# Optimization experiments

Measured on AMD Instinct MI355X. Metric: run time of the kernel, lower is better.

## Reference

```python
import jax, jax.numpy as jnp
from jax import lax
import numpy as np

D, E, N, L = 192, 384, 16, 2
P_SZ, IMG, C_IN, K = 16, 224, 3, 3
NP = (IMG // P_SZ) ** 2          # 196 patches
M = NP + 1                        # +cls token
BATCH = 8


def setup_inputs() -> dict:
    key = jax.random.key(0)
    ks = iter(jax.random.split(key, 40))
    nrm = lambda shape, s=0.02: jax.random.normal(next(ks), shape, jnp.float32) * s
    inp = {
        "img": jax.random.normal(next(ks), (BATCH, C_IN, IMG, IMG), jnp.float32),
        "patch_w": nrm((C_IN * P_SZ * P_SZ, D)),
        "patch_b": jnp.zeros((D,), jnp.float32),
        "cls": jnp.zeros((1, 1, D), jnp.float32),
        "pos": nrm((1, M, D)),
        # per-layer stacked params (leading dim L)
        "ln_g": jnp.ones((L, D), jnp.float32), "ln_b": jnp.zeros((L, D), jnp.float32),
        "Wx": nrm((L, D, E)), "bx": jnp.zeros((L, E), jnp.float32),
        "Wz": nrm((L, D, E)), "bz": jnp.zeros((L, E), jnp.float32),
        "cwf": nrm((L, E, 1, K), 0.1), "cbf": jnp.zeros((L, E), jnp.float32),
        "cwb": nrm((L, E, 1, K), 0.1), "cbb": jnp.zeros((L, E), jnp.float32),
        "WBf": nrm((L, E, E * N)), "bBf": jnp.zeros((L, E * N), jnp.float32),
        "WCf": nrm((L, E, E * N)), "bCf": jnp.zeros((L, E * N), jnp.float32),
        "WDf": jnp.zeros((L, E, E), jnp.float32), "bDf": jnp.zeros((L, E), jnp.float32),
        "Af": nrm((L, E, N), 0.01), "dbf": jnp.zeros((L, E), jnp.float32),
        "WBb": nrm((L, E, E * N)), "bBb": jnp.zeros((L, E * N), jnp.float32),
        "WCb": nrm((L, E, E * N)), "bCb": jnp.zeros((L, E * N), jnp.float32),
        "WDb": jnp.zeros((L, E, E), jnp.float32), "bDb": jnp.zeros((L, E), jnp.float32),
        "Ab": nrm((L, E, N), 0.01), "dbb": jnp.zeros((L, E), jnp.float32),
        "Wout": nrm((L, E, D)), "bout": jnp.zeros((L, D), jnp.float32),
        "ng": jnp.ones((D,), jnp.float32), "nb": jnp.zeros((D,), jnp.float32),
    }
    return inp


def layernorm(x, g, b, eps=1e-5):
    mu = x.mean(-1, keepdims=True)
    var = ((x - mu) ** 2).mean(-1, keepdims=True)
    return (x - mu) * lax.rsqrt(var + eps) * g + b


def dwconv(x, w, b):
    # x: (B, M, E), w: (E, 1, K) depthwise, 'same' padding
    xc = jnp.transpose(x, (0, 2, 1))  # (B, E, M)
    pad = (w.shape[-1] - 1) // 2
    y = lax.conv_general_dilated(xc, w, (1,), [(pad, pad)],
                                 dimension_numbers=("NCH", "OIH", "NCH"),
                                 feature_group_count=w.shape[0])
    return jnp.transpose(y, (0, 2, 1)) + b


def ssm_recurrence(A, Bm, Cm, x):
    # A,Bm,Cm: (B,M,E,N); x: (B,M,E). Log-space prefix-product scan.
    eps = 1e-6
    signA = jnp.sign(A)
    absA = jnp.clip(jnp.abs(A), eps)
    logP = jnp.cumsum(jnp.log(absA), axis=1)
    P = jnp.cumprod(signA, axis=1) * jnp.exp(logP)
    invP = 1.0 / (P + eps)
    S = jnp.cumsum(invP * Bm * x[..., None], axis=1)
    h = P * S
    return (h * Cm).sum(-1)  # (B, M, E)


def vim_block(x, p, i):
    Bsz, Mseq, _ = x.shape
    xn = layernorm(x, p["ln_g"][i], p["ln_b"][i])
    xp = xn @ p["Wx"][i] + p["bx"][i]
    z = xn @ p["Wz"][i] + p["bz"][i]
    xf = jax.nn.silu(dwconv(xp, p["cwf"][i], p["cbf"][i]))
    xb = jax.nn.silu(dwconv(xp[:, ::-1], p["cwb"][i], p["cbb"][i])[:, ::-1])

    def branch(xs, WB, bB, WC, bC, WD, bD, Apar, db):
        Bm = (xs @ WB + bB).reshape(Bsz, Mseq, E, N)
        Cm = (xs @ WC + bC).reshape(Bsz, Mseq, E, N)
        Delta = jax.nn.softplus(xs @ WD + bD + db)          # (B,M,E)
        Afull = Delta[..., None] * Apar[None, None]          # (B,M,E,N)
        Bfull = Delta[..., None] * Bm
        return ssm_recurrence(Afull, Bfull, Cm, xs)

    y_f = branch(xf, p["WBf"][i], p["bBf"][i], p["WCf"][i], p["bCf"][i],
                 p["WDf"][i], p["bDf"][i], p["Af"][i], p["dbf"][i])
    y_b = branch(xb, p["WBb"][i], p["bBb"][i], p["WCb"][i], p["bCb"][i],
                 p["WDb"][i], p["bDb"][i], p["Ab"][i], p["dbb"][i])
    g = jax.nn.silu(z)
    y = (y_f + y_b) * g
    return y @ p["Wout"][i] + p["bout"][i] + x


def reference(img, patch_w, patch_b, cls, pos, ln_g, ln_b, Wx, bx, Wz, bz,
              cwf, cbf, cwb, cbb, WBf, bBf, WCf, bCf, WDf, bDf, Af, dbf,
              WBb, bBb, WCb, bCb, WDb, bDb, Ab, dbb, Wout, bout, ng, nb):
    Bsz = img.shape[0]
    hn = IMG // P_SZ
    # patchify (equivalent to Conv2d kernel=stride=patch): (B,3,H,W)->(B,NP,3*p*p)
    patches = img.reshape(Bsz, C_IN, hn, P_SZ, hn, P_SZ)
    patches = patches.transpose(0, 2, 4, 1, 3, 5).reshape(Bsz, NP, C_IN * P_SZ * P_SZ)
    x = patches @ patch_w + patch_b                           # (B,NP,D)
    x = jnp.concatenate([jnp.broadcast_to(cls, (Bsz, 1, D)), x], axis=1)
    x = x + pos
    p = dict(ln_g=ln_g, ln_b=ln_b, Wx=Wx, bx=bx, Wz=Wz, bz=bz, cwf=cwf, cbf=cbf,
             cwb=cwb, cbb=cbb, WBf=WBf, bBf=bBf, WCf=WCf, bCf=bCf, WDf=WDf,
             bDf=bDf, Af=Af, dbf=dbf, WBb=WBb, bBb=bBb, WCb=WCb, bCb=bCb,
             WDb=WDb, bDb=bDb, Ab=Ab, dbb=dbb, Wout=Wout, bout=bout)
    for i in range(L):
        x = vim_block(x, p, i)
    return layernorm(x, ng, nb)  # (B, M, D)
```

## Files before the change

### kernel.cpp

```cpp
#include <hip/hip_runtime.h>
#include <hip/hip_bf16.h>
#include <math.h>

#define BATCH   8
#define C_IN    3
#define IMG_SZ  224
#define P_SZ    16
#define NPATCH  196
#define MSEQ    197
#define DDIM    192
#define EDIM    384
#define NSTATE  16
#define ENDIM   (EDIM*NSTATE)
#define LLAYERS 2
#define ROWS    (BATCH*MSEQ)
#define PROWS   (BATCH*NPATCH)
#define PATCH_K (C_IN*P_SZ*P_SZ)
#define AP_ROWS 1664

typedef unsigned short u16;
typedef __attribute__((ext_vector_type(8))) short bf16x8;
typedef __attribute__((ext_vector_type(16))) float f32x16;

__device__ __forceinline__ float silu_f(float x) { return x / (1.f + expf(-x)); }

__device__ __forceinline__ u16 f2bf(float f) {
    unsigned u = __float_as_uint(f);
    unsigned r = (u + 0x7FFFu + ((u >> 16) & 1u)) >> 16;
    return (u16)r;
}
__device__ __forceinline__ float bf2f(u16 h) {
    return __uint_as_float(((unsigned)h) << 16);
}

__global__ __launch_bounds__(256) void patchify_k(const float* __restrict__ img,
                                                  float* __restrict__ out) {
    int idx = blockIdx.x * 256 + threadIdx.x;
    if (idx >= PROWS * PATCH_K) return;
    int r = idx / PATCH_K, col = idx - r * PATCH_K;
    int b = r / NPATCH, p = r - b * NPATCH;
    int ph = p / 14, pw = p - ph * 14;
    int c = col >> 8, rem = col & 255, py = rem >> 4, px = rem & 15;
    out[idx] = img[((b * C_IN + c) * IMG_SZ + ph * P_SZ + py) * IMG_SZ + pw * P_SZ + px];
}

__global__ __launch_bounds__(256) void assemble_k(const float* __restrict__ xemb,
                                                  const float* __restrict__ cls,
                                                  const float* __restrict__ pos,
                                                  float* __restrict__ x) {
    int idx = blockIdx.x * 256 + threadIdx.x;
    if (idx >= ROWS * DDIM) return;
    int d = idx % DDIM;
    int bm = idx / DDIM;
    int m = bm % MSEQ, b = bm / MSEQ;
    float v;
    if (m == 0) v = cls[d];
    else        v = xemb[((b * NPATCH) + (m - 1)) * DDIM + d];
    x[idx] = v + pos[m * DDIM + d];
}

__global__ __launch_bounds__(256) void layernorm_k(const float* __restrict__ x,
                                                   const float* __restrict__ g,
                                                   const float* __restrict__ b,
                                                   float* __restrict__ o, int nrows) {
    int wave = threadIdx.x >> 6;
    int lane = threadIdx.x & 63;
    int row = blockIdx.x * 4 + wave;
    if (row >= nrows) return;
    const float* xr = x + (long)row * DDIM;
    float v0 = xr[lane], v1 = xr[lane + 64], v2 = xr[lane + 128];
    float s = v0 + v1 + v2;
    #pragma unroll
    for (int off = 1; off < 64; off <<= 1) s += __shfl_xor(s, off);
    float mu = s * (1.f / 192.f);
    float d0 = v0 - mu, d1 = v1 - mu, d2 = v2 - mu;
    float q = d0 * d0 + d1 * d1 + d2 * d2;
    #pragma unroll
    for (int off = 1; off < 64; off <<= 1) q += __shfl_xor(q, off);
    float inv = rsqrtf(q * (1.f / 192.f) + 1e-5f);
    float* orow = o + (long)row * DDIM;
    orow[lane]       = d0 * inv * g[lane]       + b[lane];
    orow[lane + 64]  = d1 * inv * g[lane + 64]  + b[lane + 64];
    orow[lane + 128] = d2 * inv * g[lane + 128] + b[lane + 128];
}

__global__ __launch_bounds__(256) void convA_k(const float* __restrict__ xf,
                                               const float* __restrict__ xb,
                                               u16* __restrict__ Af3,
                                               u16* __restrict__ Ab3) {
    int idx = blockIdx.x * 256 + threadIdx.x;
    if (idx >= ROWS * EDIM) return;
    int row = idx / EDIM, k = idx - row * EDIM;
    long base = (long)row * EDIM + k;
    #pragma unroll
    for (int s = 0; s < 2; ++s) {
        float x = s ? xb[idx] : xf[idx];
        u16* out = s ? Ab3 : Af3;
        u16 hb = f2bf(x);        float fh = bf2f(hb);
        float r1 = x - fh;
        u16 mb = f2bf(r1);       float fm = bf2f(mb);
        u16 lb = f2bf(r1 - fm);
        out[base] = hb;
        out[(long)AP_ROWS * EDIM + base] = mb;
        out[2L * AP_ROWS * EDIM + base] = lb;
    }
}

__global__ __launch_bounds__(256) void convWt_k(const float* __restrict__ W0,
                                                const float* __restrict__ W1,
                                                const float* __restrict__ W2,
                                                const float* __restrict__ W3,
                                                u16* __restrict__ Wt) {
    int z = blockIdx.z;
    const float* W = (z == 0) ? W0 : (z == 1) ? W1 : (z == 2) ? W2 : W3;
    u16* out = Wt + (long)z * 3L * ENDIM * EDIM;
    __shared__ float tile[64][65];
    int n0 = blockIdx.x * 64, k0 = blockIdx.y * 64;
    int t = threadIdx.x;
    #pragma unroll
    for (int i = 0; i < 16; ++i) {
        int id = t + 256 * i;
        int kk = id >> 6, nn = id & 63;
        tile[kk][nn] = W[(long)(k0 + kk) * ENDIM + n0 + nn];
    }
    __syncthreads();
    #pragma unroll
    for (int i = 0; i < 2; ++i) {
        int id = t + 256 * i;
        int nn = id >> 3, ch = id & 7;
        uint4 hq, mq, lq;
        u16* hp = (u16*)&hq; u16* mp = (u16*)&mq; u16* lp = (u16*)&lq;
        #pragma unroll
        for (int j = 0; j < 8; ++j) {
            float x = tile[ch * 8 + j][nn];
            u16 hb = f2bf(x);        float fh = bf2f(hb);
            float r1 = x - fh;
            u16 mb = f2bf(r1);       float fm = bf2f(mb);
            u16 lb = f2bf(r1 - fm);
            hp[j] = hb; mp[j] = mb; lp[j] = lb;
        }
        long rowoff = (long)(n0 + nn) * EDIM + k0 + ch * 8;
        *(uint4*)&out[rowoff] = hq;
        *(uint4*)&out[(long)ENDIM * EDIM + rowoff] = mq;
        *(uint4*)&out[2L * ENDIM * EDIM + rowoff] = lq;
    }
}

__global__ __launch_bounds__(256) void gemm_mfma(
        const u16* __restrict__ A3,
        const u16* __restrict__ Wt0, const float* __restrict__ b0, float* __restrict__ C0,
        const u16* __restrict__ Wt1, const float* __restrict__ b1, float* __restrict__ C1) {
    const u16* Wt    = blockIdx.z ? Wt1 : Wt0;
    const float* bias = blockIdx.z ? b1 : b0;
    float* C          = blockIdx.z ? C1 : C0;
    __shared__ u16 As[3][128][40];
    int t = threadIdx.x;
    int lane = t & 63, wv = t >> 6;
    int wr = wv >> 1, wc = wv & 1;
    int l31 = lane & 31, l5 = lane >> 5;
    int rowBase = blockIdx.y * 128;
    long colBase = (long)blockIdx.x * 128;
    f32x16 acc[2][2] = {};

    for (int k0 = 0; k0 < EDIM; k0 += 32) {
        #pragma unroll
        for (int i = 0; i < 6; ++i) {
            int id = t + 256 * i;
            int p = id >> 9, rem = id & 511, row = rem >> 2, ch = rem & 3;
            const u16* src = A3 + ((long)p * AP_ROWS + rowBase + row) * EDIM + k0 + ch * 8;
            uint4 v = *(const uint4*)src;
            *(uint4*)&As[p][row][ch * 8] = v;
        }
        __syncthreads();
        bf16x8 af[2][2][3], wf[2][2][3];
        #pragma unroll
        for (int ks = 0; ks < 2; ++ks) {
            #pragma unroll
            for (int r = 0; r < 2; ++r)
                #pragma unroll
                for (int p = 0; p < 3; ++p)
                    af[ks][r][p] = *(const bf16x8*)&As[p][wr * 64 + r * 32 + l31][ks * 16 + l5 * 8];
            #pragma unroll
            for (int c = 0; c < 2; ++c)
                #pragma unroll
                for (int p = 0; p < 3; ++p)
                    wf[ks][c][p] = *(const bf16x8*)&Wt[((long)p * ENDIM + colBase + wc * 64 + c * 32 + l31) * EDIM
                                                      + k0 + ks * 16 + l5 * 8];
        }
        #pragma unroll
        for (int ks = 0; ks < 2; ++ks)
            #pragma unroll
            for (int r = 0; r < 2; ++r)
                #pragma unroll
                for (int c = 0; c < 2; ++c) {
                    f32x16 d = acc[r][c];
                    d = __builtin_amdgcn_mfma_f32_32x32x16_bf16(af[ks][r][0], wf[ks][c][0], d, 0, 0, 0);
                    d = __builtin_amdgcn_mfma_f32_32x32x16_bf16(af[ks][r][0], wf[ks][c][1], d, 0, 0, 0);
                    d = __builtin_amdgcn_mfma_f32_32x32x16_bf16(af[ks][r][1], wf[ks][c][0], d, 0, 0, 0);
                    d = __builtin_amdgcn_mfma_f32_32x32x16_bf16(af[ks][r][0], wf[ks][c][2], d, 0, 0, 0);
                    d = __builtin_amdgcn_mfma_f32_32x32x16_bf16(af[ks][r][2], wf[ks][c][0], d, 0, 0, 0);
                    d = __builtin_amdgcn_mfma_f32_32x32x16_bf16(af[ks][r][1], wf[ks][c][1], d, 0, 0, 0);
                    acc[r][c] = d;
                }
        __syncthreads();
    }
    #pragma unroll
    for (int r = 0; r < 2; ++r) {
        int rb = rowBase + wr * 64 + r * 32 + 4 * l5;
        #pragma unroll
        for (int c = 0; c < 2; ++c) {
            long cb = colBase + wc * 64 + c * 32 + l31;
            float bv = bias[cb];
            #pragma unroll
            for (int i = 0; i < 16; ++i) {
                int rr = rb + (i & 3) + 8 * (i >> 2);
                if (rr < ROWS) C[(long)rr * ENDIM + cb] = acc[r][c][i] + bv;
            }
        }
    }
}

#define SBK 16
template<bool SP, bool HASB2, bool HASRES>
__global__ __launch_bounds__(64) void gemm_s(const float* __restrict__ A0,
                                             const float* __restrict__ W0,
                                             const float* __restrict__ b10,
                                             const float* __restrict__ b20,
                                             const float* __restrict__ r0,
                                             float* __restrict__ C0,
                                             const float* __restrict__ A1,
                                             const float* __restrict__ W1,
                                             const float* __restrict__ b11,
                                             const float* __restrict__ b21,
                                             const float* __restrict__ r1,
                                             float* __restrict__ C1,
                                             int M, int N, int K) {
    const float* A  = blockIdx.z ? A1  : A0;
    const float* W  = blockIdx.z ? W1  : W0;
    const float* bp = blockIdx.z ? b11 : b10;
    const float* b2 = blockIdx.z ? b21 : b20;
    const float* rp = blockIdx.z ? r1  : r0;
    float*       C  = blockIdx.z ? C1  : C0;
    __shared__ float As[2][SBK][36];
    __shared__ float Wsh[2][SBK][36];
    int t = threadIdx.x;
    int tx = t & 7, ty = t >> 3;
    int rowBase = blockIdx.y * 32;
    long colBase = (long)blockIdx.x * 32;
    int rA = t >> 2, kqA = (t & 3) << 2;
    int kW = t >> 3, nqW = (t & 7) << 2;
    float acc[4][4] = {};
    int r0i = rowBase + rA, r1i = r0i + 16;

    auto loadA = [&](int k0, float4& a0, float4& a1) {
        a0 = make_float4(0.f,0.f,0.f,0.f); a1 = a0;
        if (r0i < M) a0 = *(const float4*)&A[(long)r0i * K + k0 + kqA];
        if (r1i < M) a1 = *(const float4*)&A[(long)r1i * K + k0 + kqA];
    };
    auto stage = [&](int buf, float4 a0, float4 a1, float4 w0, float4 w1) {
        As[buf][kqA + 0][rA] = a0.x; As[buf][kqA + 1][rA] = a0.y;
        As[buf][kqA + 2][rA] = a0.z; As[buf][kqA + 3][rA] = a0.w;
        As[buf][kqA + 0][rA + 16] = a1.x; As[buf][kqA + 1][rA + 16] = a1.y;
        As[buf][kqA + 2][rA + 16] = a1.z; As[buf][kqA + 3][rA + 16] = a1.w;
        *(float4*)&Wsh[buf][kW][nqW]     = w0;
        *(float4*)&Wsh[buf][kW + 8][nqW] = w1;
    };
    auto compute = [&](int buf) {
        #pragma unroll
        for (int kk = 0; kk < SBK; ++kk) {
            float4 av = *(const float4*)&As[buf][kk][ty << 2];
            float4 wv = *(const float4*)&Wsh[buf][kk][tx << 2];
            float ar[4] = {av.x, av.y, av.z, av.w};
            float wr[4] = {wv.x, wv.y, wv.z, wv.w};
            #pragma unroll
            for (int i = 0; i < 4; ++i)
                #pragma unroll
                for (int j = 0; j < 4; ++j) acc[i][j] += ar[i] * wr[j];
        }
    };

    {
        float4 a0, a1;
        loadA(0, a0, a1);
        float4 w0 = *(const float4*)&W[(long)kW * N + colBase + nqW];
        float4 w1 = *(const float4*)&W[(long)(kW + 8) * N + colBase + nqW];
        stage(0, a0, a1, w0, w1);
    }
    __syncthreads();
    int cur = 0;
    int nt = K / SBK;
    for (int kt = 1; kt < nt; ++kt) {
        int k0 = kt * SBK;
        float4 a0, a1;
        loadA(k0, a0, a1);
        float4 w0 = *(const float4*)&W[(long)(k0 + kW) * N + colBase + nqW];
        float4 w1 = *(const float4*)&W[(long)(k0 + kW + 8) * N + colBase + nqW];
        compute(cur);
        stage(cur ^ 1, a0, a1, w0, w1);
        __syncthreads();
        cur ^= 1;
    }
    compute(cur);

    #pragma unroll
    for (int i = 0; i < 4; ++i) {
        int r = rowBase + (ty << 2) + i;
        if (r >= M) break;
        long cb = colBase + (tx << 2);
        float vv[4];
        #pragma unroll
        for (int j = 0; j < 4; ++j) {
            float v = acc[i][j] + bp[cb + j];
            if (HASB2) v += b2[cb + j];
            if (SP) {
                double vd = (double)v;
                v = (float)(log1p(exp(-fabs(vd))) + fmax(vd, 0.0));
            }
            if (HASRES) v += rp[(long)r * N + cb + j];
            vv[j] = v;
        }
        float4 o; o.x = vv[0]; o.y = vv[1]; o.z = vv[2]; o.w = vv[3];
        *(float4*)&C[(long)r * N + cb] = o;
    }
}

__global__ __launch_bounds__(256) void dwconv_k(const float* __restrict__ xp,
                                                const float* __restrict__ wf,
                                                const float* __restrict__ bf,
                                                const float* __restrict__ wb,
                                                const float* __restrict__ bb,
                                                float* __restrict__ xf,
                                                float* __restrict__ xb) {
    int idx = blockIdx.x * 256 + threadIdx.x;
    if (idx >= ROWS * EDIM) return;
    int e = idx % EDIM;
    int bm = idx / EDIM;
    int m = bm % MSEQ, b = bm / MSEQ;
    const float* base = xp + (long)b * MSEQ * EDIM + e;
    float xm1 = (m > 0)        ? base[(m - 1) * EDIM] : 0.f;
    float x0  =                  base[m * EDIM];
    float xp1 = (m < MSEQ - 1) ? base[(m + 1) * EDIM] : 0.f;
    float f = wf[e * 3 + 0] * xm1 + wf[e * 3 + 1] * x0 + wf[e * 3 + 2] * xp1 + bf[e];
    float r = wb[e * 3 + 0] * xp1 + wb[e * 3 + 1] * x0 + wb[e * 3 + 2] * xm1 + bb[e];
    xf[idx] = silu_f(f);
    xb[idx] = silu_f(r);
}

__global__ __launch_bounds__(256) void ssm_scan_k(const float* __restrict__ Bm,
                                                  const float* __restrict__ Cm,
                                                  const float* __restrict__ Dlt,
                                                  const float* __restrict__ xs,
                                                  const float* __restrict__ Apar,
                                                  float* __restrict__ y,
                                                  const float* __restrict__ yother,
                                                  const float* __restrict__ zg,
                                                  float* __restrict__ ycomb) {
#pragma clang fp contract(off)
    __shared__ float lgP[MSEQ][17];
    __shared__ float trm[MSEQ][17];
    __shared__ signed char sgn[MSEQ][17];
    int be = blockIdx.x;
    int b = be / EDIM, e = be - b * EDIM;
    int t = threadIdx.x;
    int n0 = t & 15;
    float Ap = Apar[e * NSTATE + n0];
    const long dxBase = (long)b * MSEQ * EDIM + e;
    const long bcBase = (long)b * MSEQ * ENDIM + e * NSTATE;

    for (int idx = t; idx < MSEQ * NSTATE; idx += 256) {
        int m = idx >> 4;
        float delta = Dlt[dxBase + (long)m * EDIM];
        float A = delta * Ap;
        float sa = (A > 0.f) ? 1.f : ((A < 0.f) ? -1.f : 0.f);
        float absA = fmaxf(fabsf(A), 1e-6f);
        lgP[m][n0] = (float)log((double)absA);
        sgn[m][n0] = (signed char)sa;
    }
    __syncthreads();
    if (t < NSTATE) {
        float cl = 0.f, cs = 1.f;
        for (int m = 0; m < MSEQ; ++m) {
            float sa = (float)sgn[m][t];
            cs = cs * sa;
            cl = cl + lgP[m][t];
            lgP[m][t] = cl;
            sgn[m][t] = (signed char)cs;
        }
    }
    __syncthreads();
    for (int idx = t; idx < MSEQ * NSTATE; idx += 256) {
        int m = idx >> 4;
        float cl = lgP[m][n0];
        float cs = (float)sgn[m][n0];
        float ex = (float)exp((double)cl);
        float P = cs * ex;
        float tt = P + 1e-6f;
        float invP = 1.0f / tt;
        float delta = Dlt[dxBase + (long)m * EDIM];
        float xv = xs[dxBase + (long)m * EDIM];
        float Bv = Bm[bcBase + (long)m * ENDIM + n0];
        float Bfull = delta * Bv;
        float t1 = invP * Bfull;
        float t2 = t1 * xv;
        trm[m][n0] = t2;
        lgP[m][n0] = P;
    }
    __syncthreads();
    if (t < NSTATE) {
        float S = 0.f;
        for (int m = 0; m < MSEQ; ++m) {
            S = S + trm[m][t];
            float h = lgP[m][t] * S;
            trm[m][t] = h;
        }
    }
    __syncthreads();
    for (int m = t; m < MSEQ; m += 256) {
        const float* cp = &Cm[bcBase + (long)m * ENDIM];
        float a[16];
        #pragma unroll
        for (int n = 0; n < 16; ++n) a[n] = trm[m][n] * cp[n];
        float b0 = a[0] + a[8],  b1 = a[1] + a[9];
        float b2v = a[2] + a[10], b3 = a[3] + a[11];
        float b4 = a[4] + a[12], b5 = a[5] + a[13];
        float b6 = a[6] + a[14], b7 = a[7] + a[15];
        float c0 = b0 + b1, c2 = b2v + b3, c4 = b4 + b5, c6 = b6 + b7;
        float d0 = c0 + c2, d4 = c4 + c6;
        float val = d0 + d4;
        long o = dxBase + (long)m * EDIM;
        if (ycomb) ycomb[o] = (yother[o] + val) * silu_f(zg[o]);
        else       y[o] = val;
    }
}

extern "C" void kernel_launch(void* const* d_in, const int* in_sizes, int n_in,
                              void* d_out, int out_size, void* d_ws, size_t ws_size,
                              hipStream_t stream) {
    const float* img     = (const float*)d_in[0];
    const float* patch_w = (const float*)d_in[1];
    const float* patch_b = (const float*)d_in[2];
    const float* cls     = (const float*)d_in[3];
    const float* pos     = (const float*)d_in[4];
    const float* ln_g    = (const float*)d_in[5];
    const float* ln_b    = (const float*)d_in[6];
    const float* Wx  = (const float*)d_in[7];  const float* bx  = (const float*)d_in[8];
    const float* Wz  = (const float*)d_in[9];  const float* bz  = (const float*)d_in[10];
    const float* cwf = (const float*)d_in[11]; const float* cbf = (const float*)d_in[12];
    const float* cwb = (const float*)d_in[13]; const float* cbb = (const float*)d_in[14];
    const float* WBf = (const float*)d_in[15]; const float* bBf = (const float*)d_in[16];
    const float* WCf = (const float*)d_in[17]; const float* bCf = (const float*)d_in[18];
    const float* WDf = (const float*)d_in[19]; const float* bDf = (const float*)d_in[20];
    const float* Af  = (const float*)d_in[21]; const float* dbf = (const float*)d_in[22];
    const float* WBb = (const float*)d_in[23]; const float* bBb = (const float*)d_in[24];
    const float* WCb = (const float*)d_in[25]; const float* bCb = (const float*)d_in[26];
    const float* WDb = (const float*)d_in[27]; const float* bDb = (const float*)d_in[28];
    const float* Ab  = (const float*)d_in[29]; const float* dbb = (const float*)d_in[30];
    const float* Wout= (const float*)d_in[31]; const float* bout= (const float*)d_in[32];
    const float* ng  = (const float*)d_in[33]; const float* nb  = (const float*)d_in[34];

    float* ws = (float*)d_ws;
    float* xA   = ws;
    float* xB   = xA  + (size_t)ROWS * DDIM;
    float* xn   = xB  + (size_t)ROWS * DDIM;
    float* xp   = xn  + (size_t)ROWS * DDIM;
    float* zb   = xp  + (size_t)ROWS * EDIM;
    float* xfb  = zb  + (size_t)ROWS * EDIM;
    float* xbb  = xfb + (size_t)ROWS * EDIM;
    float* yfb  = xbb + (size_t)ROWS * EDIM;
    float* ybb  = yfb + (size_t)ROWS * EDIM;
    float* ycb  = ybb + (size_t)ROWS * EDIM;
    float* dlt  = ycb + (size_t)ROWS * EDIM;
    float* dlt2 = dlt + (size_t)ROWS * EDIM;
    float* Bmb  = dlt2 + (size_t)ROWS * EDIM;
    float* Cmb  = Bmb + (size_t)ROWS * ENDIM;
    u16*   Af3  = (u16*)(Cmb + (size_t)ROWS * ENDIM);
    u16*   Ab3  = Af3 + 3L * AP_ROWS * EDIM;
    u16*   Wt4  = Ab3 + 3L * AP_ROWS * EDIM;
    float* patches = Bmb;
    float* xemb    = Bmb + (size_t)PROWS * PATCH_K;

    const long WtSz = 3L * ENDIM * EDIM;

    patchify_k<<<(PROWS * PATCH_K + 255) / 256, 256, 0, stream>>>(img, patches);
    {
        dim3 g(DDIM / 32, (PROWS + 31) / 32, 1);
        gemm_s<false, false, false><<<g, 64, 0, stream>>>(
            patches, patch_w, patch_b, nullptr, nullptr, xemb,
            patches, patch_w, patch_b, nullptr, nullptr, xemb,
            PROWS, DDIM, PATCH_K);
    }
    assemble_k<<<(ROWS * DDIM + 255) / 256, 256, 0, stream>>>(xemb, cls, pos, xA);

    float* cur = xA; float* nxt = xB;
    for (int i = 0; i < LLAYERS; ++i) {
        layernorm_k<<<(ROWS + 3) / 4, 256, 0, stream>>>(cur, ln_g + i * DDIM, ln_b + i * DDIM, xn, ROWS);
        {
            dim3 g(EDIM / 32, (ROWS + 31) / 32, 2);
            gemm_s<false, false, false><<<g, 64, 0, stream>>>(
                xn, Wx + (size_t)i * DDIM * EDIM, bx + i * EDIM, nullptr, nullptr, xp,
                xn, Wz + (size_t)i * DDIM * EDIM, bz + i * EDIM, nullptr, nullptr, zb,
                ROWS, EDIM, DDIM);
        }
        dwconv_k<<<(ROWS * EDIM + 255) / 256, 256, 0, stream>>>(xp, cwf + i * EDIM * 3, cbf + i * EDIM,
                                                                cwb + i * EDIM * 3, cbb + i * EDIM, xfb, xbb);
        convA_k<<<(ROWS * EDIM + 255) / 256, 256, 0, stream>>>(xfb, xbb, Af3, Ab3);
        {
            dim3 g(EDIM / 32, (ROWS + 31) / 32, 2);
            gemm_s<true, true, false><<<g, 64, 0, stream>>>(
                xfb, WDf + (size_t)i * EDIM * EDIM, bDf + i * EDIM, dbf + i * EDIM, nullptr, dlt,
                xbb, WDb + (size_t)i * EDIM * EDIM, bDb + i * EDIM, dbb + i * EDIM, nullptr, dlt2,
                ROWS, EDIM, EDIM);
        }
        {
            dim3 g(ENDIM / 64, EDIM / 64, 4);
            convWt_k<<<g, 256, 0, stream>>>(
                WBf + (size_t)i * EDIM * ENDIM, WCf + (size_t)i * EDIM * ENDIM,
                WBb + (size_t)i * EDIM * ENDIM, WCb + (size_t)i * EDIM * ENDIM, Wt4);
        }
        {
            dim3 g(ENDIM / 128, AP_ROWS / 128, 2);
            gemm_mfma<<<g, 256, 0, stream>>>(
                Af3,
                Wt4 + 0 * WtSz, bBf + i * ENDIM, Bmb,
                Wt4 + 1 * WtSz, bCf + i * ENDIM, Cmb);
        }
        ssm_scan_k<<<BATCH * EDIM, 256, 0, stream>>>(Bmb, Cmb, dlt, xfb, Af + i * EDIM * NSTATE,
                                                     yfb, nullptr, nullptr, nullptr);
        {
            dim3 g(ENDIM / 128, AP_ROWS / 128, 2);
            gemm_mfma<<<g, 256, 0, stream>>>(
                Ab3,
                Wt4 + 2 * WtSz, bBb + i * ENDIM, Bmb,
                Wt4 + 3 * WtSz, bCb + i * ENDIM, Cmb);
        }
        ssm_scan_k<<<BATCH * EDIM, 256, 0, stream>>>(Bmb, Cmb, dlt2, xbb, Ab + i * EDIM * NSTATE,
                                                     ybb, yfb, zb, ycb);
        {
            dim3 g(DDIM / 32, (ROWS + 31) / 32, 1);
            gemm_s<false, false, true><<<g, 64, 0, stream>>>(
                ycb, Wout + (size_t)i * EDIM * DDIM, bout + i * DDIM, nullptr, cur, nxt,
                ycb, Wout + (size_t)i * EDIM * DDIM, bout + i * DDIM, nullptr, cur, nxt,
                ROWS, DDIM, EDIM);
        }
        float* t = cur; cur = nxt; nxt = t;
    }
    layernorm_k<<<(ROWS + 3) / 4, 256, 0, stream>>>(cur, ng, nb, (float*)d_out, ROWS);
}
```

Measured before the change: 1.115 ms.

## Pre-swizzle bf16x3 operands into MFMA fragment layout and drop LDS staging

The split bf16 operand buffers for A and W are now written directly in per-lane MFMA fragment order (32-row by 16-k blocks of 512 elements). The GEMM then loads each fragment with one contiguous 16-byte read per lane from global memory, removing the shared-memory staging of A and both barriers per k-step. The conversion kernels now pack eight values per thread and zero-fill padding rows. The risk is that the GEMM now relies entirely on global and L2 bandwidth, with no LDS reuse of A across waves and no explicit prefetch.

```diff
diff --git a/kernel.cpp b/kernel.cpp
--- a/kernel.cpp
+++ b/kernel.cpp
@@ -17,6 +17,10 @@
 #define PROWS   (BATCH*NPATCH)
 #define PATCH_K (C_IN*P_SZ*P_SZ)
 #define AP_ROWS 1664
+#define MFRAGS  52
+#define NFRAGS  192
+#define KBLKS   24
+#define FRAG    512
 
 typedef unsigned short u16;
 typedef __attribute__((ext_vector_type(8))) short bf16x8;
@@ -89,20 +93,35 @@
                                                u16* __restrict__ Af3,
                                                u16* __restrict__ Ab3) {
     int idx = blockIdx.x * 256 + threadIdx.x;
-    if (idx >= ROWS * EDIM) return;
-    int row = idx / EDIM, k = idx - row * EDIM;
-    long base = (long)row * EDIM + k;
+    if (idx >= MFRAGS * KBLKS * 64) return;
+    int lane = idx & 63;
+    int kb = (idx >> 6) % KBLKS;
+    int mf = idx / (64 * KBLKS);
+    int row = mf * 32 + (lane & 31);
+    int k = kb * 16 + (lane >> 5) * 8;
+    long fo = ((long)mf * KBLKS + kb) * FRAG + (long)lane * 8;
+    const long plane = (long)MFRAGS * KBLKS * FRAG;
     #pragma unroll
     for (int s = 0; s < 2; ++s) {
-        float x = s ? xb[idx] : xf[idx];
+        const float* src = s ? xb : xf;
         u16* out = s ? Ab3 : Af3;
-        u16 hb = f2bf(x);        float fh = bf2f(hb);
-        float r1 = x - fh;
-        u16 mb = f2bf(r1);       float fm = bf2f(mb);
-        u16 lb = f2bf(r1 - fm);
-        out[base] = hb;
-        out[(long)AP_ROWS * EDIM + base] = mb;
-        out[2L * AP_ROWS * EDIM + base] = lb;
+        uint4 hq = {0,0,0,0}, mq = {0,0,0,0}, lq = {0,0,0,0};
+        if (row < ROWS) {
+            u16* hp = (u16*)&hq; u16* mp = (u16*)&mq; u16* lp = (u16*)&lq;
+            const float* xr = src + (long)row * EDIM + k;
+            #pragma unroll
+            for (int j = 0; j < 8; ++j) {
+                float x = xr[j];
+                u16 hb = f2bf(x);        float fh = bf2f(hb);
+                float r1 = x - fh;
+                u16 mb = f2bf(r1);       float fm = bf2f(mb);
+                u16 lb = f2bf(r1 - fm);
+                hp[j] = hb; mp[j] = mb; lp[j] = lb;
+            }
+        }
+        *(uint4*)&out[fo] = hq;
+        *(uint4*)&out[plane + fo] = mq;
+        *(uint4*)&out[2 * plane + fo] = lq;
     }
 }
 
@@ -113,7 +132,8 @@
                                                 u16* __restrict__ Wt) {
     int z = blockIdx.z;
     const float* W = (z == 0) ? W0 : (z == 1) ? W1 : (z == 2) ? W2 : W3;
-    u16* out = Wt + (long)z * 3L * ENDIM * EDIM;
+    const long plane = (long)NFRAGS * KBLKS * FRAG;
+    u16* out = Wt + (long)z * 3L * plane;
     __shared__ float tile[64][65];
     int n0 = blockIdx.x * 64, k0 = blockIdx.y * 64;
     int t = threadIdx.x;
@@ -128,6 +148,10 @@
     for (int i = 0; i < 2; ++i) {
         int id = t + 256 * i;
         int nn = id >> 3, ch = id & 7;
+        int n = n0 + nn;
+        int kc = k0 + ch * 8;
+        int nf = n >> 5, l31 = n & 31;
+        int kb = kc >> 4, l5 = (kc >> 3) & 1;
         uint4 hq, mq, lq;
         u16* hp = (u16*)&hq; u16* mp = (u16*)&mq; u16* lp = (u16*)&lq;
         #pragma unroll
@@ -139,10 +163,10 @@
             u16 lb = f2bf(r1 - fm);
             hp[j] = hb; mp[j] = mb; lp[j] = lb;
         }
-        long rowoff = (long)(n0 + nn) * EDIM + k0 + ch * 8;
-        *(uint4*)&out[rowoff] = hq;
-        *(uint4*)&out[(long)ENDIM * EDIM + rowoff] = mq;
-        *(uint4*)&out[2L * ENDIM * EDIM + rowoff] = lq;
+        long fo = ((long)nf * KBLKS + kb) * FRAG + (long)(l5 * 32 + l31) * 8;
+        *(uint4*)&out[fo] = hq;
+        *(uint4*)&out[plane + fo] = mq;
+        *(uint4*)&out[2 * plane + fo] = lq;
     }
 }
 
@@ -150,60 +174,47 @@
         const u16* __restrict__ A3,
         const u16* __restrict__ Wt0, const float* __restrict__ b0, float* __restrict__ C0,
         const u16* __restrict__ Wt1, const float* __restrict__ b1, float* __restrict__ C1) {
-    const u16* Wt    = blockIdx.z ? Wt1 : Wt0;
+    const u16* Wt     = blockIdx.z ? Wt1 : Wt0;
     const float* bias = blockIdx.z ? b1 : b0;
     float* C          = blockIdx.z ? C1 : C0;
-    __shared__ u16 As[3][128][40];
     int t = threadIdx.x;
     int lane = t & 63, wv = t >> 6;
     int wr = wv >> 1, wc = wv & 1;
     int l31 = lane & 31, l5 = lane >> 5;
+    int mf0 = blockIdx.y * 4 + wr * 2;
+    int nf0 = blockIdx.x * 4 + wc * 2;
+    const u16* Ab = A3 + (long)lane * 8;
+    const u16* Wb = Wt + (long)lane * 8;
+    f32x16 acc[2][2] = {};
+
+    for (int kb = 0; kb < KBLKS; ++kb) {
+        bf16x8 af[2][3], wf[2][3];
+        #pragma unroll
+        for (int r = 0; r < 2; ++r)
+            #pragma unroll
+            for (int p = 0; p < 3; ++p)
+                af[r][p] = *(const bf16x8*)(Ab + (((long)p * MFRAGS + mf0 + r) * KBLKS + kb) * FRAG);
+        #pragma unroll
+        for (int c = 0; c < 2; ++c)
+            #pragma unroll
+            for (int p = 0; p < 3; ++p)
+                wf[c][p] = *(const bf16x8*)(Wb + (((long)p * NFRAGS + nf0 + c) * KBLKS + kb) * FRAG);
+        #pragma unroll
+        for (int r = 0; r < 2; ++r)
+            #pragma unroll
+            for (int c = 0; c < 2; ++c) {
+                f32x16 d = acc[r][c];
+                d = __builtin_amdgcn_mfma_f32_32x32x16_bf16(af[r][0], wf[c][0], d, 0, 0, 0);
+                d = __builtin_amdgcn_mfma_f32_32x32x16_bf16(af[r][0], wf[c][1], d, 0, 0, 0);
+                d = __builtin_amdgcn_mfma_f32_32x32x16_bf16(af[r][1], wf[c][0], d, 0, 0, 0);
+                d = __builtin_amdgcn_mfma_f32_32x32x16_bf16(af[r][0], wf[c][2], d, 0, 0, 0);
+                d = __builtin_amdgcn_mfma_f32_32x32x16_bf16(af[r][2], wf[c][0], d, 0, 0, 0);
+                d = __builtin_amdgcn_mfma_f32_32x32x16_bf16(af[r][1], wf[c][1], d, 0, 0, 0);
+                acc[r][c] = d;
+            }
+    }
     int rowBase = blockIdx.y * 128;
     long colBase = (long)blockIdx.x * 128;
-    f32x16 acc[2][2] = {};
-
-    for (int k0 = 0; k0 < EDIM; k0 += 32) {
-        #pragma unroll
-        for (int i = 0; i < 6; ++i) {
-            int id = t + 256 * i;
-            int p = id >> 9, rem = id & 511, row = rem >> 2, ch = rem & 3;
-            const u16* src = A3 + ((long)p * AP_ROWS + rowBase + row) * EDIM + k0 + ch * 8;
-            uint4 v = *(const uint4*)src;
-            *(uint4*)&As[p][row][ch * 8] = v;
-        }
-        __syncthreads();
-        bf16x8 af[2][2][3], wf[2][2][3];
-        #pragma unroll
-        for (int ks = 0; ks < 2; ++ks) {
-            #pragma unroll
-            for (int r = 0; r < 2; ++r)
-                #pragma unroll
-                for (int p = 0; p < 3; ++p)
-                    af[ks][r][p] = *(const bf16x8*)&As[p][wr * 64 + r * 32 + l31][ks * 16 + l5 * 8];
-            #pragma unroll
-            for (int c = 0; c < 2; ++c)
-                #pragma unroll
-                for (int p = 0; p < 3; ++p)
-                    wf[ks][c][p] = *(const bf16x8*)&Wt[((long)p * ENDIM + colBase + wc * 64 + c * 32 + l31) * EDIM
-                                                      + k0 + ks * 16 + l5 * 8];
-        }
-        #pragma unroll
-        for (int ks = 0; ks < 2; ++ks)
-            #pragma unroll
-            for (int r = 0; r < 2; ++r)
-                #pragma unroll
-                for (int c = 0; c < 2; ++c) {
-                    f32x16 d = acc[r][c];
-                    d = __builtin_amdgcn_mfma_f32_32x32x16_bf16(af[ks][r][0], wf[ks][c][0], d, 0, 0, 0);
-                    d = __builtin_amdgcn_mfma_f32_32x32x16_bf16(af[ks][r][0], wf[ks][c][1], d, 0, 0, 0);
-                    d = __builtin_amdgcn_mfma_f32_32x32x16_bf16(af[ks][r][1], wf[ks][c][0], d, 0, 0, 0);
-                    d = __builtin_amdgcn_mfma_f32_32x32x16_bf16(af[ks][r][0], wf[ks][c][2], d, 0, 0, 0);
-                    d = __builtin_amdgcn_mfma_f32_32x32x16_bf16(af[ks][r][2], wf[ks][c][0], d, 0, 0, 0);
-                    d = __builtin_amdgcn_mfma_f32_32x32x16_bf16(af[ks][r][1], wf[ks][c][1], d, 0, 0, 0);
-                    acc[r][c] = d;
-                }
-        __syncthreads();
-    }
     #pragma unroll
     for (int r = 0; r < 2; ++r) {
         int rb = rowBase + wr * 64 + r * 32 + 4 * l5;
@@ -474,12 +485,12 @@
     float* Bmb  = dlt2 + (size_t)ROWS * EDIM;
     float* Cmb  = Bmb + (size_t)ROWS * ENDIM;
     u16*   Af3  = (u16*)(Cmb + (size_t)ROWS * ENDIM);
-    u16*   Ab3  = Af3 + 3L * AP_ROWS * EDIM;
-    u16*   Wt4  = Ab3 + 3L * AP_ROWS * EDIM;
+    u16*   Ab3  = Af3 + 3L * MFRAGS * KBLKS * FRAG;
+    u16*   Wt4  = Ab3 + 3L * MFRAGS * KBLKS * FRAG;
     float* patches = Bmb;
     float* xemb    = Bmb + (size_t)PROWS * PATCH_K;
 
-    const long WtSz = 3L * ENDIM * EDIM;
+    const long WtSz = 3L * NFRAGS * KBLKS * FRAG;
 
     patchify_k<<<(PROWS * PATCH_K + 255) / 256, 256, 0, stream>>>(img, patches);
     {
@@ -503,7 +514,7 @@
         }
         dwconv_k<<<(ROWS * EDIM + 255) / 256, 256, 0, stream>>>(xp, cwf + i * EDIM * 3, cbf + i * EDIM,
                                                                 cwb + i * EDIM * 3, cbb + i * EDIM, xfb, xbb);
-        convA_k<<<(ROWS * EDIM + 255) / 256, 256, 0, stream>>>(xfb, xbb, Af3, Ab3);
+        convA_k<<<(MFRAGS * KBLKS * 64 + 255) / 256, 256, 0, stream>>>(xfb, xbb, Af3, Ab3);
         {
             dim3 g(EDIM / 32, (ROWS + 31) / 32, 2);
             gemm_s<true, true, false><<<g, 64, 0, stream>>>(
```

New measurement: 933.0 us. 1.2x faster.
